# Kernel optimization log

Measured on AMD Instinct MI355X. Metric: run time of the kernel, lower is better.

The kernel has to match this reference:

```python
import jax, jax.numpy as jnp
import numpy as np

B, L, DM = 4, 2048, 1024
NL, ED, N, DTR, DCONV, SEGN = 2, 2048, 2, 64, 2, 8
SEG = max(8, round(L / SEGN))  # 256, L divisible -> all segments full


def setup_inputs():
    key = jax.random.key(0)
    ks = jax.random.split(key, 12)
    def nrm(k, sh, sc=0.02):
        return jax.random.normal(k, sh, jnp.float32) * sc
    return {
        "x": nrm(ks[0], (B, L, DM), 1.0),
        "rms_w": jnp.ones((NL, DM), jnp.float32),
        "in_w": nrm(ks[1], (NL, 2 * ED, DM)),
        "c1_w": nrm(ks[2], (NL, ED, DCONV), 0.5),
        "c1_b": jnp.zeros((NL, ED), jnp.float32),
        "c2_w": nrm(ks[3], (NL, ED, DCONV), 0.5),
        "c2_b": jnp.zeros((NL, ED), jnp.float32),
        "xp_w": nrm(ks[4], (NL, DTR + N, ED)),
        "dt_w": nrm(ks[5], (NL, ED, DTR)),
        "dt_b": jax.random.uniform(ks[6], (NL, ED), jnp.float32, -5.0, -3.0),
        "A_log": jnp.tile(jnp.log(jnp.arange(1, N + 1, dtype=jnp.float32)), (NL, ED, 1)),
        "Dp": jnp.ones((NL, ED), jnp.float32),
        "out_w": nrm(ks[7], (NL, DM, ED)),
        "k1_w": nrm(ks[8], (NL, 3 * ED, ED)),
        "k1_b": jnp.zeros((NL, 3 * ED), jnp.float32),
        "k2_w": nrm(ks[9], (NL, ED, 3 * ED)),
        "k3_w": nrm(ks[10], (NL, ED, ED)),
        "ln_g": jnp.ones((NL, ED), jnp.float32),
        "ln_b": jnp.zeros((NL, ED), jnp.float32),
        "k_alpha": jnp.zeros((NL, ED), jnp.float32),
        "sigma": jnp.full((NL,), 0.5, jnp.float32),
    }


def _dwconv(x, w, b):
    # causal depthwise conv, kernel DCONV: torch Conv1d(groups=ED, padding=DCONV-1)[..., :L]
    Lx = x.shape[1]
    xp = jnp.pad(x, ((0, 0), (DCONV - 1, 0), (0, 0)))
    y = b
    for k in range(DCONV):
        y = y + xp[:, k:k + Lx, :] * w[:, k]
    return y


def _fdu(x, dt, sigma):
    # Fourier differentiation over time axis (B, T, D)
    T = x.shape[1]
    f = jnp.fft.fftfreq(T).astype(jnp.float32)[None, :, None]
    Xf = jnp.fft.fft(x, axis=1)
    g = jnp.exp(-(f ** 2) * sigma ** 2)
    omega = 2j * jnp.pi * f / (dt + 1e-5)
    return jnp.fft.ifft(omega * (Xf * g), axis=1).real


def _kproj(e, w1, b1, w2, w3, g, bb):
    h = jax.nn.relu(e @ w1.T + b1)
    h = jax.nn.relu(h @ w2.T)
    h = h @ w3.T
    mu = jnp.mean(h, -1, keepdims=True)
    v = jnp.mean((h - mu) ** 2, -1, keepdims=True)
    return g * (h - mu) * jax.lax.rsqrt(v + 1e-5) + bb


def _pscan(a, b):
    # h_t = a_t * h_{t-1} + b_t, h_0 = b_0; (B, Lseg, ED, N)
    def comb(l, r):
        return (r[0] * l[0], r[0] * l[1] + r[1])
    return jax.lax.associative_scan(comb, (a, b), axis=1)[1]


def reference(x, rms_w, in_w, c1_w, c1_b, c2_w, c2_b, xp_w, dt_w, dt_b,
              A_log, Dp, out_w, k1_w, k1_b, k2_w, k3_w, ln_g, ln_b, k_alpha, sigma):
    h = x
    for i in range(NL):
        # RMSNorm
        xn = h * jax.lax.rsqrt(jnp.mean(h ** 2, -1, keepdims=True) + 1e-5) * rms_w[i]
        xz = xn @ in_w[i].T
        xs, z = xz[..., :ED], xz[..., ED:]
        xs = _dwconv(xs, c1_w[i], c1_b[i])
        xs = _dwconv(xs, c2_w[i], c2_b[i])
        xs = jax.nn.silu(xs)
        # ssm projections
        A = -jnp.exp(A_log[i])                       # (ED, N)
        dC = xs @ xp_w[i].T
        dr, C = dC[..., :DTR], dC[..., DTR:]
        delta = jax.nn.softplus(dr @ dt_w[i].T + dt_b[i])
        alpha = jnp.clip(k_alpha[i], 0.01, 0.99)
        yh = jnp.zeros((B, SEG, ED), xs.dtype)
        K = jnp.zeros((B, SEG, ED), xs.dtype)
        hs = []
        for s0 in range(0, L, SEG):
            xg = xs[:, s0:s0 + SEG]
            dg = delta[:, s0:s0 + SEG]
            Cg = C[:, s0:s0 + SEG]
            Kerr = jax.nn.soft_sign((xg - yh) ** 2)
            Knew = _kproj(Kerr, k1_w[i], k1_b[i], k2_w[i], k3_w[i], ln_g[i], ln_b[i])
            K = (1.0 - alpha) * K + alpha * Knew
            Kdy = K * _fdu(xg, dg, sigma[i])
            # SSOL: A_k = (A - KCA)(1 + KC), B_k = -(A - KCA) K
            Ku = K[..., None]                        # (B, Lseg, ED, 1)
            KC = Ku * Cg[:, :, None, :]              # (B, Lseg, ED, N)
            AmK = A - KC * A
            A_k = AmK * (1.0 + KC)
            B_k = -AmK * Ku
            dA = jnp.exp(dg[..., None] * A_k)
            dBx = dg[..., None] * B_k * xg[..., None] + Kdy[..., None]
            hseg = _pscan(dA, dBx)
            yh = jnp.einsum('blen,bln->ble', hseg, Cg) + Dp[i] * xg
            hs.append(hseg)
        hsall = jnp.concatenate(hs, axis=1)          # (B, L, ED, N)
        y = jnp.einsum('blen,bln->ble', hsall, C) + Dp[i] * xs
        out = (y * jax.nn.silu(z)) @ out_w[i].T
        h = h + out
    return h
```

## Files before the change

kernel.cpp:

```cpp
#include <hip/hip_runtime.h>
#include <stdint.h>


#define B_    4
#define L_    2048
#define DM_   1024
#define ED_   2048
#define SEG_  256
#define NSEG_ 8
#define CH_   16
#define TS_   16

typedef _Float16 f16x8 __attribute__((ext_vector_type(8)));
typedef _Float16 f16x4 __attribute__((ext_vector_type(4)));
typedef float    f32x4 __attribute__((ext_vector_type(4)));

__device__ __forceinline__ float siluf(float x)     { return x / (1.0f + expf(-x)); }
__device__ __forceinline__ float softplusf(float x) { return (x > 20.0f) ? x : log1pf(expf(x)); }

__global__ void f2h_kernel(const float* __restrict__ in, _Float16* __restrict__ out, int n4) {
    int i = blockIdx.x * 256 + threadIdx.x;
    if (i < n4) {
        float4 v = ((const float4*)in)[i];
        f16x4 h;
        h[0] = (_Float16)v.x; h[1] = (_Float16)v.y;
        h[2] = (_Float16)v.z; h[3] = (_Float16)v.w;
        ((f16x4*)out)[i] = h;
    }
}

__global__ __launch_bounds__(256) void rmsnorm_k(const float* __restrict__ H,
                                                 const float* __restrict__ w,
                                                 _Float16* __restrict__ out) {
    __shared__ float sred[4];
    int row = blockIdx.x;
    const float* h = H + (size_t)row * DM_;
    float ss = 0.f;
    for (int c = threadIdx.x; c < DM_; c += 256) { float v = h[c]; ss += v * v; }
    for (int off = 32; off; off >>= 1) ss += __shfl_down(ss, off, 64);
    if ((threadIdx.x & 63) == 0) sred[threadIdx.x >> 6] = ss;
    __syncthreads();
    float tot = sred[0] + sred[1] + sred[2] + sred[3];
    float scale = rsqrtf(tot * (1.0f / DM_) + 1e-5f);
    for (int c = threadIdx.x; c < DM_; c += 256)
        out[(size_t)row * DM_ + c] = (_Float16)(h[c] * scale * w[c]);
}

template<int BM, int BN, int WR, int WC, int EPI>
__global__ __launch_bounds__(256, 2)
void gemm_nt(const _Float16* __restrict__ A, const _Float16* __restrict__ Bw,
             int K, int N,
             float* outf, _Float16* __restrict__ outh, _Float16* __restrict__ outh2,
             const float* __restrict__ bias, const float* addsrc) {
    constexpr int WTM = BM / (16 * WR);
    constexpr int WTN = BN / (16 * WC);
    constexpr int NA = BM * 4 / 256;
    constexpr int NB = BN * 4 / 256;
    static_assert(BM * 4 % 256 == 0 && BN * 4 % 256 == 0, "tile");

    __shared__ __align__(16) _Float16 lsA[BM * 32];
    __shared__ __align__(16) _Float16 lsB[BN * 32];

    const int tid  = threadIdx.x;
    const int lane = tid & 63;
    const int wid  = tid >> 6;
    const int wm   = wid / WC, wn = wid % WC;
    const int m0   = blockIdx.y * BM, n0 = blockIdx.x * BN;

    f32x4 acc[WTM][WTN];
#pragma unroll
    for (int i = 0; i < WTM; ++i)
#pragma unroll
        for (int j = 0; j < WTN; ++j) acc[i][j] = (f32x4){0.f, 0.f, 0.f, 0.f};

    for (int k0 = 0; k0 < K; k0 += 32) {
        f16x8 ra[NA], rb[NB];
#pragma unroll
        for (int it = 0; it < NA; ++it) {
            int c = tid + 256 * it;
            int row = c >> 2, q = c & 3;
            int kc = q ^ ((row >> 1) & 3);
            ra[it] = *(const f16x8*)(A + (size_t)(m0 + row) * K + k0 + kc * 8);
        }
#pragma unroll
        for (int it = 0; it < NB; ++it) {
            int c = tid + 256 * it;
            int row = c >> 2, q = c & 3;
            int kc = q ^ ((row >> 1) & 3);
            rb[it] = *(const f16x8*)(Bw + (size_t)(n0 + row) * K + k0 + kc * 8);
        }
        __syncthreads();
#pragma unroll
        for (int it = 0; it < NA; ++it) { int c = tid + 256 * it; *(f16x8*)&lsA[c * 8] = ra[it]; }
#pragma unroll
        for (int it = 0; it < NB; ++it) { int c = tid + 256 * it; *(f16x8*)&lsB[c * 8] = rb[it]; }
        __syncthreads();

        f16x8 af[WTM], bfr[WTN];
#pragma unroll
        for (int i = 0; i < WTM; ++i) {
            int row = wm * (WTM * 16) + i * 16 + (lane & 15);
            int q = (lane >> 4) ^ ((row >> 1) & 3);
            af[i] = *(const f16x8*)&lsA[row * 32 + q * 8];
        }
#pragma unroll
        for (int j = 0; j < WTN; ++j) {
            int row = wn * (WTN * 16) + j * 16 + (lane & 15);
            int q = (lane >> 4) ^ ((row >> 1) & 3);
            bfr[j] = *(const f16x8*)&lsB[row * 32 + q * 8];
        }
#pragma unroll
        for (int i = 0; i < WTM; ++i)
#pragma unroll
            for (int j = 0; j < WTN; ++j)
                acc[i][j] = __builtin_amdgcn_mfma_f32_16x16x32_f16(af[i], bfr[j], acc[i][j], 0, 0, 0);
    }

#pragma unroll
    for (int i = 0; i < WTM; ++i) {
#pragma unroll
        for (int j = 0; j < WTN; ++j) {
            int mb = m0 + wm * (WTM * 16) + i * 16 + ((lane >> 4) * 4);
            int nb = n0 + wn * (WTN * 16) + j * 16 + (lane & 15);
#pragma unroll
            for (int r = 0; r < 4; ++r) {
                float v = acc[i][j][r];
                int m = mb + r;
                size_t o = (size_t)m * N + nb;
                if (EPI == 0) {
                    outf[o] = v;
                } else if (EPI == 1) {
                    int half = N >> 1;
                    if (nb < half) outh [(size_t)m * half + nb]          = (_Float16)v;
                    else           outh2[(size_t)m * half + (nb - half)] = (_Float16)v;
                } else if (EPI == 2) {
                    v += bias[nb]; v = fmaxf(v, 0.f); outh[o] = (_Float16)v;
                } else if (EPI == 3) {
                    v = fmaxf(v, 0.f); outh[o] = (_Float16)v;
                } else if (EPI == 4) {
                    outf[o] = addsrc[o] + v;
                }
            }
        }
    }
}

__global__ void convsilu_k(const _Float16* __restrict__ xp,
                           const float* __restrict__ c1w, const float* __restrict__ c1b,
                           const float* __restrict__ c2w, const float* __restrict__ c2b,
                           _Float16* __restrict__ xs, int layer) {
    size_t idx = (size_t)blockIdx.x * 256 + threadIdx.x;
    int e = (int)(idx % ED_);
    size_t bl = idx / ED_;
    int l = (int)(bl % L_);
    size_t wb = (size_t)layer * ED_ + e;
    float w10 = c1w[wb * 2], w11 = c1w[wb * 2 + 1], b1 = c1b[wb];
    float w20 = c2w[wb * 2], w21 = c2w[wb * 2 + 1], b2 = c2b[wb];
    float x0  = (float)xp[idx];
    float xm1 = (l >= 1) ? (float)xp[idx - ED_] : 0.f;
    float xm2 = (l >= 2) ? (float)xp[idx - 2 * ED_] : 0.f;
    float s1  = b1 + w10 * xm1 + w11 * x0;
    float s1m = (l >= 1) ? (b1 + w10 * xm2 + w11 * xm1) : 0.f;
    float s2  = b2 + w20 * s1m + w21 * s1;
    xs[idx] = (_Float16)siluf(s2);
}

__global__ __launch_bounds__(256) void gemv_dc(const _Float16* __restrict__ xs,
                                               const float* __restrict__ xp_w,
                                               float* __restrict__ dC, int layer) {
    int row  = blockIdx.x * 4 + (threadIdx.x >> 6);
    int lane = threadIdx.x & 63;
    const _Float16* xr = xs + (size_t)row * ED_;
    float xrow[32];
#pragma unroll
    for (int c = 0; c < 32; ++c) xrow[c] = (float)xr[c * 64 + lane];
    const float* W = xp_w + (size_t)layer * 66 * ED_;
    for (int j = 0; j < 66; ++j) {
        const float* wj = W + (size_t)j * ED_;
        float p = 0.f;
#pragma unroll
        for (int c = 0; c < 32; ++c) p += xrow[c] * wj[c * 64 + lane];
        for (int off = 32; off; off >>= 1) p += __shfl_down(p, off, 64);
        if (lane == 0) dC[(size_t)row * 66 + j] = p;
    }
}

__global__ __launch_bounds__(256) void delta_k(const float* __restrict__ dC,
                                               const float* __restrict__ dt_w,
                                               const float* __restrict__ dt_b,
                                               _Float16* __restrict__ delta, int layer) {
    __shared__ float dr[64];
    int row = blockIdx.y;
    int col = blockIdx.x * 256 + threadIdx.x;
    if (threadIdx.x < 64) dr[threadIdx.x] = dC[(size_t)row * 66 + threadIdx.x];
    __syncthreads();
    const float* w = dt_w + ((size_t)layer * ED_ + col) * 64;
    float acc = dt_b[(size_t)layer * ED_ + col];
#pragma unroll
    for (int k = 0; k < 64; k += 4) {
        float4 wv = *(const float4*)&w[k];
        acc += dr[k] * wv.x + dr[k + 1] * wv.y + dr[k + 2] * wv.z + dr[k + 3] * wv.w;
    }
    delta[(size_t)row * ED_ + col] = (_Float16)softplusf(acc);
}

__global__ void kerr_k(const _Float16* __restrict__ xs, const _Float16* __restrict__ y,
                       _Float16* __restrict__ kerr, int s0) {
    size_t idx = (size_t)blockIdx.x * 256 + threadIdx.x;
    int e = (int)(idx % ED_);
    size_t bt = idx / ED_;
    int t = (int)(bt % SEG_);
    int b = (int)(bt / SEG_);
    size_t gx = ((size_t)(b * L_ + s0 + t)) * ED_ + e;
    float xg = (float)xs[gx];
    float yh = (s0 == 0) ? 0.f : (float)y[gx - (size_t)SEG_ * ED_];
    float d = xg - yh;
    float s = d * d;
    kerr[idx] = (_Float16)(s / (1.f + s));
}

__global__ __launch_bounds__(256) void ln_ema_k(const float* __restrict__ h3,
                                                const float* __restrict__ ln_g,
                                                const float* __restrict__ ln_b,
                                                const float* __restrict__ k_alpha,
                                                float* __restrict__ K, int layer) {
    __shared__ float sred[4];
    int row = blockIdx.x;
    const float* hr = h3 + (size_t)row * ED_;
    float s = 0.f;
    for (int c = threadIdx.x; c < ED_; c += 256) s += hr[c];
    for (int off = 32; off; off >>= 1) s += __shfl_down(s, off, 64);
    if ((threadIdx.x & 63) == 0) sred[threadIdx.x >> 6] = s;
    __syncthreads();
    float mu = (sred[0] + sred[1] + sred[2] + sred[3]) * (1.0f / ED_);
    __syncthreads();
    float v = 0.f;
    for (int c = threadIdx.x; c < ED_; c += 256) { float d = hr[c] - mu; v += d * d; }
    for (int off = 32; off; off >>= 1) v += __shfl_down(v, off, 64);
    if ((threadIdx.x & 63) == 0) sred[threadIdx.x >> 6] = v;
    __syncthreads();
    float var = (sred[0] + sred[1] + sred[2] + sred[3]) * (1.0f / ED_);
    float rstd = rsqrtf(var + 1e-5f);
    for (int c = threadIdx.x; c < ED_; c += 256) {
        size_t wb = (size_t)layer * ED_ + c;
        float kn = ln_g[wb] * (hr[c] - mu) * rstd + ln_b[wb];
        float al = fminf(fmaxf(k_alpha[wb], 0.01f), 0.99f);
        size_t ki = (size_t)row * ED_ + c;
        K[ki] = (1.f - al) * K[ki] + al * kn;
    }
}

__global__ __launch_bounds__(256) void fdu_kdy_k(const _Float16* __restrict__ xs,
                                                 const _Float16* __restrict__ delta,
                                                 const float* __restrict__ K,
                                                 float* __restrict__ Kdy,
                                                 const float* __restrict__ sigma,
                                                 int layer, int s0) {
    __shared__ float re[SEG_ * 16];
    __shared__ float im[SEG_ * 16];
    __shared__ float twc[128], tws[128];
    const int tid = threadIdx.x;
    const int b   = blockIdx.x >> 7;
    const int e0  = (blockIdx.x & 127) * 16;
    float sg = sigma[layer];
    float sg2 = sg * sg;
    if (tid < 128) {
        float ang = -6.283185307179586f * (float)tid * (1.0f / 256.0f);
        twc[tid] = cosf(ang);
        tws[tid] = sinf(ang);
    }
    for (int ii = tid; ii < SEG_ * 16; ii += 256) {
        int t = ii >> 4, el = ii & 15;
        re[ii] = (float)xs[((size_t)(b * L_ + s0 + t)) * ED_ + e0 + el];
        im[ii] = 0.f;
    }
    __syncthreads();
    const int bb = tid >> 4;
    const int el = tid & 15;
#pragma unroll
    for (int ls = 7; ls >= 0; --ls) {
        int span = 1 << ls;
#pragma unroll
        for (int bi = 0; bi < 8; ++bi) {
            int bidx = bb + (bi << 4);
            int j    = bidx & (span - 1);
            int grp  = bidx >> ls;
            int p    = (grp << (ls + 1)) + j;
            int twi  = j << (7 - ls);
            int i0   = (p << 4) + el;
            int i1   = i0 + (span << 4);
            float ur = re[i0], ui = im[i0];
            float vr = re[i1], vi = im[i1];
            re[i0] = ur + vr; im[i0] = ui + vi;
            float dr = ur - vr, di = ui - vi;
            float c = twc[twi], sn = tws[twi];
            re[i1] = dr * c - di * sn;
            im[i1] = dr * sn + di * c;
        }
        __syncthreads();
    }
    for (int ii = tid; ii < SEG_ * 16; ii += 256) {
        int p = ii >> 4, ee = ii & 15;
        int k = __brev((unsigned)p) >> 24;
        float f = ((k < 128) ? (float)k : (float)(k - 256)) * (1.0f / 256.0f);
        float dt = (float)delta[((size_t)(b * L_ + s0 + k)) * ED_ + e0 + ee];
        float q = 6.283185307179586f * f * expf(-f * f * sg2) / (dt + 1e-5f);
        float xr = re[ii], xi = im[ii];
        re[ii] = -q * xi;
        im[ii] =  q * xr;
    }
    __syncthreads();
#pragma unroll
    for (int ls = 0; ls <= 7; ++ls) {
        int span = 1 << ls;
#pragma unroll
        for (int bi = 0; bi < 8; ++bi) {
            int bidx = bb + (bi << 4);
            int j    = bidx & (span - 1);
            int grp  = bidx >> ls;
            int p    = (grp << (ls + 1)) + j;
            int twi  = j << (7 - ls);
            int i0   = (p << 4) + el;
            int i1   = i0 + (span << 4);
            float c = twc[twi], sn = -tws[twi];
            float vr = re[i1], vi = im[i1];
            float tr = vr * c - vi * sn;
            float ti = vr * sn + vi * c;
            float ur = re[i0], ui = im[i0];
            re[i0] = ur + tr; im[i0] = ui + ti;
            re[i1] = ur - tr; im[i1] = ui - ti;
        }
        __syncthreads();
    }
    for (int ii = tid; ii < SEG_ * 16; ii += 256) {
        int t = ii >> 4, ee = ii & 15;
        size_t ki = ((size_t)(b * SEG_ + t)) * ED_ + e0 + ee;
        Kdy[ki] = K[ki] * re[ii] * (1.0f / 256.0f);
    }
}

__device__ __forceinline__ void scan_coefs(float dg, float xg, float Kt, float kdy,
                                           float C0, float C1, float A0, float A1,
                                           float& dA0, float& dB0, float& dA1, float& dB1) {
    float KC0 = Kt * C0;
    float AmK0 = A0 * (1.f - KC0);
    float Ak0 = AmK0 * (1.f + KC0);
    float Bk0 = -AmK0 * Kt;
    dA0 = expf(dg * Ak0);
    dB0 = dg * Bk0 * xg + kdy;
    float KC1 = Kt * C1;
    float AmK1 = A1 * (1.f - KC1);
    float Ak1 = AmK1 * (1.f + KC1);
    float Bk1 = -AmK1 * Kt;
    dA1 = expf(dg * Ak1);
    dB1 = dg * Bk1 * xg + kdy;
}

__global__ void scanA_k(const _Float16* __restrict__ delta, const _Float16* __restrict__ xs,
                        const float* __restrict__ K, const float* __restrict__ Kdy,
                        const float* __restrict__ dC, const float* __restrict__ A_log,
                        float* __restrict__ P0, float* __restrict__ P1,
                        float* __restrict__ S0, float* __restrict__ S1,
                        int layer, int s0) {
    int e = blockIdx.x * 256 + threadIdx.x;
    int b = blockIdx.y >> 4;
    int c = blockIdx.y & 15;
    float A0 = -expf(A_log[((size_t)layer * ED_ + e) * 2 + 0]);
    float A1 = -expf(A_log[((size_t)layer * ED_ + e) * 2 + 1]);
    float p0 = 1.f, p1 = 1.f, s0v = 0.f, s1v = 0.f;
    for (int tt = 0; tt < TS_; ++tt) {
        int t = c * TS_ + tt;
        size_t gi = ((size_t)(b * L_ + s0 + t)) * ED_ + e;
        size_t ki = ((size_t)(b * SEG_ + t)) * ED_ + e;
        float dg = (float)delta[gi], xg = (float)xs[gi];
        float Kt = K[ki], kdy = Kdy[ki];
        size_t ci = (size_t)(b * L_ + s0 + t) * 66 + 64;
        float C0 = dC[ci], C1 = dC[ci + 1];
        float dA0, dB0, dA1, dB1;
        scan_coefs(dg, xg, Kt, kdy, C0, C1, A0, A1, dA0, dB0, dA1, dB1);
        p0 *= dA0; s0v = dA0 * s0v + dB0;
        p1 *= dA1; s1v = dA1 * s1v + dB1;
    }
    size_t si = ((size_t)(b * CH_ + c)) * ED_ + e;
    P0[si] = p0; P1[si] = p1; S0[si] = s0v; S1[si] = s1v;
}

__global__ void scanB_k(const float* __restrict__ P0, const float* __restrict__ P1,
                        const float* __restrict__ S0, const float* __restrict__ S1,
                        float* __restrict__ Ca0, float* __restrict__ Ca1) {
    int t = blockIdx.x * 256 + threadIdx.x;
    int b = t / ED_, e = t % ED_;
    float h0 = 0.f, h1 = 0.f;
    for (int c = 0; c < CH_; ++c) {
        size_t si = ((size_t)(b * CH_ + c)) * ED_ + e;
        Ca0[si] = h0; Ca1[si] = h1;
        h0 = P0[si] * h0 + S0[si];
        h1 = P1[si] * h1 + S1[si];
    }
}

__global__ void scanC_k(const _Float16* __restrict__ delta, const _Float16* __restrict__ xs,
                        const float* __restrict__ K, const float* __restrict__ Kdy,
                        const float* __restrict__ dC, const float* __restrict__ A_log,
                        const float* __restrict__ Dp,
                        const float* __restrict__ Ca0, const float* __restrict__ Ca1,
                        _Float16* __restrict__ y, int layer, int s0) {
    int e = blockIdx.x * 256 + threadIdx.x;
    int b = blockIdx.y >> 4;
    int c = blockIdx.y & 15;
    float A0 = -expf(A_log[((size_t)layer * ED_ + e) * 2 + 0]);
    float A1 = -expf(A_log[((size_t)layer * ED_ + e) * 2 + 1]);
    float Dpe = Dp[(size_t)layer * ED_ + e];
    size_t si = ((size_t)(b * CH_ + c)) * ED_ + e;
    float h0 = Ca0[si], h1 = Ca1[si];
    for (int tt = 0; tt < TS_; ++tt) {
        int t = c * TS_ + tt;
        size_t gi = ((size_t)(b * L_ + s0 + t)) * ED_ + e;
        size_t ki = ((size_t)(b * SEG_ + t)) * ED_ + e;
        float dg = (float)delta[gi], xg = (float)xs[gi];
        float Kt = K[ki], kdy = Kdy[ki];
        size_t ci = (size_t)(b * L_ + s0 + t) * 66 + 64;
        float C0 = dC[ci], C1 = dC[ci + 1];
        float dA0, dB0, dA1, dB1;
        scan_coefs(dg, xg, Kt, kdy, C0, C1, A0, A1, dA0, dB0, dA1, dB1);
        h0 = dA0 * h0 + dB0;
        h1 = dA1 * h1 + dB1;
        y[gi] = (_Float16)(h0 * C0 + h1 * C1 + Dpe * xg);
    }
}

__global__ void gate_k(const _Float16* __restrict__ y, const _Float16* __restrict__ z,
                       _Float16* __restrict__ g) {
    size_t idx = (size_t)blockIdx.x * 256 + threadIdx.x;
    g[idx] = (_Float16)((float)y[idx] * siluf((float)z[idx]));
}

#define OFF_WK1   ((size_t)0)
#define OFF_WK2   (OFF_WK1 + 25165824)
#define OFF_WK3   (OFF_WK2 + 25165824)
#define OFF_WOUT  (OFF_WK3 + 8388608)
#define OFF_WIN   (OFF_WOUT + 4194304)
#define OFF_XN    (OFF_WIN + 8388608)
#define OFF_P     (OFF_XN + 16777216)
#define OFF_XS    (OFF_P + 33554432)
#define OFF_Z     (OFF_XS + 33554432)
#define OFF_Y     (OFF_Z + 33554432)
#define OFF_DC    (OFF_Y + 33554432)
#define OFF_H2    (OFF_DC + 2162688)
#define OFF_K     (OFF_H2 + 4194304)
#define OFF_KDY   (OFF_K + 8388608)
#define OFF_SP0   (OFF_KDY + 8388608)
#define OFF_SP1   (OFF_SP0 + 524288)
#define OFF_SS0   (OFF_SP1 + 524288)
#define OFF_SS1   (OFF_SS0 + 524288)
#define OFF_SC0   (OFF_SS1 + 524288)
#define OFF_SC1   (OFF_SC0 + 524288)
#define WS_NEED   (OFF_SC1 + 524288)

extern "C" void kernel_launch(void* const* d_in, const int* in_sizes, int n_in,
                              void* d_out, int out_size, void* d_ws, size_t ws_size,
                              hipStream_t stream) {
    if (ws_size < WS_NEED) return;

    const float* x_in   = (const float*)d_in[0];
    const float* rms_w  = (const float*)d_in[1];
    const float* in_w   = (const float*)d_in[2];
    const float* c1_w   = (const float*)d_in[3];
    const float* c1_b   = (const float*)d_in[4];
    const float* c2_w   = (const float*)d_in[5];
    const float* c2_b   = (const float*)d_in[6];
    const float* xp_w   = (const float*)d_in[7];
    const float* dt_w   = (const float*)d_in[8];
    const float* dt_b   = (const float*)d_in[9];
    const float* A_log  = (const float*)d_in[10];
    const float* Dp     = (const float*)d_in[11];
    const float* out_w  = (const float*)d_in[12];
    const float* k1_w   = (const float*)d_in[13];
    const float* k1_b   = (const float*)d_in[14];
    const float* k2_w   = (const float*)d_in[15];
    const float* k3_w   = (const float*)d_in[16];
    const float* ln_g   = (const float*)d_in[17];
    const float* ln_b   = (const float*)d_in[18];
    const float* k_alph = (const float*)d_in[19];
    const float* sigma  = (const float*)d_in[20];

    char* ws = (char*)d_ws;
    _Float16* w_k1  = (_Float16*)(ws + OFF_WK1);
    _Float16* w_k2  = (_Float16*)(ws + OFF_WK2);
    _Float16* w_k3  = (_Float16*)(ws + OFF_WK3);
    _Float16* w_out = (_Float16*)(ws + OFF_WOUT);
    _Float16* w_in  = (_Float16*)(ws + OFF_WIN);
    float*    h3buf = (float*)(ws + OFF_WIN);
    _Float16* xnbf  = (_Float16*)(ws + OFF_XN);
    _Float16* kerrb = (_Float16*)(ws + OFF_XN);
    _Float16* h1bf  = (_Float16*)(ws + OFF_XN + 4194304);
    _Float16* xs_pre= (_Float16*)(ws + OFF_P);
    _Float16* xsbuf = (_Float16*)(ws + OFF_XS);
    _Float16* zbuf  = (_Float16*)(ws + OFF_Z);
    _Float16* ybuf  = (_Float16*)(ws + OFF_Y);
    float*    dCbuf = (float*)(ws + OFF_DC);
    _Float16* h2bf  = (_Float16*)(ws + OFF_H2);
    float*    Kbuf  = (float*)(ws + OFF_K);
    float*    Kdybuf= (float*)(ws + OFF_KDY);
    float* sP0 = (float*)(ws + OFF_SP0);
    float* sP1 = (float*)(ws + OFF_SP1);
    float* sS0 = (float*)(ws + OFF_SS0);
    float* sS1 = (float*)(ws + OFF_SS1);
    float* sC0 = (float*)(ws + OFF_SC0);
    float* sC1 = (float*)(ws + OFF_SC1);
    float* dout = (float*)d_out;
    _Float16* delta = xs_pre;
    _Float16* gated = xs_pre;

    for (int layer = 0; layer < 2; ++layer) {
        hipMemsetAsync(Kbuf, 0, (size_t)B_ * SEG_ * ED_ * 4, stream);

        f2h_kernel<<<4096, 256, 0, stream>>>(in_w  + (size_t)layer * 4194304,  w_in,  1048576);
        f2h_kernel<<<12288, 256, 0, stream>>>(k1_w + (size_t)layer * 12582912, w_k1,  3145728);
        f2h_kernel<<<12288, 256, 0, stream>>>(k2_w + (size_t)layer * 12582912, w_k2,  3145728);
        f2h_kernel<<<4096, 256, 0, stream>>>(k3_w  + (size_t)layer * 4194304,  w_k3,  1048576);
        f2h_kernel<<<2048, 256, 0, stream>>>(out_w + (size_t)layer * 2097152,  w_out, 524288);

        const float* Hsrc = (layer == 0) ? x_in : dout;
        rmsnorm_k<<<B_ * L_, 256, 0, stream>>>(Hsrc, rms_w + (size_t)layer * DM_, xnbf);

        gemm_nt<128, 128, 2, 2, 1><<<dim3(32, 64), 256, 0, stream>>>(
            xnbf, w_in, 1024, 4096, nullptr, xs_pre, zbuf, nullptr, nullptr);

        convsilu_k<<<65536, 256, 0, stream>>>(xs_pre, c1_w, c1_b, c2_w, c2_b, xsbuf, layer);

        gemv_dc<<<2048, 256, 0, stream>>>(xsbuf, xp_w, dCbuf, layer);

        delta_k<<<dim3(8, 8192), 256, 0, stream>>>(dCbuf, dt_w, dt_b, delta, layer);

        for (int s = 0; s < NSEG_; ++s) {
            int s0 = s * SEG_;
            kerr_k<<<8192, 256, 0, stream>>>(xsbuf, ybuf, kerrb, s0);
            gemm_nt<128, 128, 2, 2, 2><<<dim3(48, 8), 256, 0, stream>>>(
                kerrb, w_k1, 2048, 6144, nullptr, h1bf, nullptr,
                k1_b + (size_t)layer * 6144, nullptr);
            gemm_nt<64, 128, 1, 4, 3><<<dim3(16, 16), 256, 0, stream>>>(
                h1bf, w_k2, 6144, 2048, nullptr, h2bf, nullptr, nullptr, nullptr);
            gemm_nt<64, 128, 1, 4, 0><<<dim3(16, 16), 256, 0, stream>>>(
                h2bf, w_k3, 2048, 2048, h3buf, nullptr, nullptr, nullptr, nullptr);
            ln_ema_k<<<B_ * SEG_, 256, 0, stream>>>(h3buf, ln_g, ln_b, k_alph, Kbuf, layer);
            fdu_kdy_k<<<B_ * (ED_ / 16), 256, 0, stream>>>(xsbuf, delta, Kbuf, Kdybuf,
                                                           sigma, layer, s0);
            scanA_k<<<dim3(ED_ / 256, B_ * CH_), 256, 0, stream>>>(
                delta, xsbuf, Kbuf, Kdybuf, dCbuf, A_log, sP0, sP1, sS0, sS1, layer, s0);
            scanB_k<<<(B_ * ED_) / 256, 256, 0, stream>>>(sP0, sP1, sS0, sS1, sC0, sC1);
            scanC_k<<<dim3(ED_ / 256, B_ * CH_), 256, 0, stream>>>(
                delta, xsbuf, Kbuf, Kdybuf, dCbuf, A_log, Dp, sC0, sC1, ybuf, layer, s0);
        }

        gate_k<<<65536, 256, 0, stream>>>(ybuf, zbuf, gated);
        gemm_nt<128, 128, 2, 2, 4><<<dim3(8, 64), 256, 0, stream>>>(
            gated, w_out, 2048, 1024, dout, nullptr, nullptr, nullptr,
            (layer == 0) ? x_in : dout);
    }
    (void)in_sizes; (void)n_in; (void)out_size;
}
```

Baseline: 5.573 ms.

## Use direct global-to-LDS loads in GEMM and move delta projection to MFMA GEMM

The GEMM main loop now uses global_load_lds to copy tiles straight into shared memory instead of staging them through registers. The scalar delta_k kernel is replaced by an fp16 MFMA GEMM with a new bias+softplus epilogue. gemv_dc now also writes an fp16 copy of the dt rank projection, and dt_w is converted to fp16 each layer. Removing register staging drops the register round trip but also loses the overlap of loads with the preceding compute, since there is still no double buffering. The delta path now runs in fp16 with slightly lower precision.

Result: faster. 4.846 ms (-13.0%).

```diff
diff --git a/kernel.cpp b/kernel.cpp
--- a/kernel.cpp
+++ b/kernel.cpp
@@ -17,6 +17,11 @@
 
 __device__ __forceinline__ float siluf(float x)     { return x / (1.0f + expf(-x)); }
 __device__ __forceinline__ float softplusf(float x) { return (x > 20.0f) ? x : log1pf(expf(x)); }
+
+#define GLD16(gptr, lptr)                                                     \
+    __builtin_amdgcn_global_load_lds(                                         \
+        (const __attribute__((address_space(1))) void*)(gptr),                \
+        (__attribute__((address_space(3))) void*)(lptr), 16, 0, 0)
 
 __global__ void f2h_kernel(const float* __restrict__ in, _Float16* __restrict__ out, int n4) {
     int i = blockIdx.x * 256 + threadIdx.x;
@@ -74,26 +79,21 @@
         for (int j = 0; j < WTN; ++j) acc[i][j] = (f32x4){0.f, 0.f, 0.f, 0.f};
 
     for (int k0 = 0; k0 < K; k0 += 32) {
-        f16x8 ra[NA], rb[NB];
+        __syncthreads();
 #pragma unroll
         for (int it = 0; it < NA; ++it) {
             int c = tid + 256 * it;
             int row = c >> 2, q = c & 3;
             int kc = q ^ ((row >> 1) & 3);
-            ra[it] = *(const f16x8*)(A + (size_t)(m0 + row) * K + k0 + kc * 8);
+            GLD16(A + (size_t)(m0 + row) * K + k0 + kc * 8, &lsA[c * 8]);
         }
 #pragma unroll
         for (int it = 0; it < NB; ++it) {
             int c = tid + 256 * it;
             int row = c >> 2, q = c & 3;
             int kc = q ^ ((row >> 1) & 3);
-            rb[it] = *(const f16x8*)(Bw + (size_t)(n0 + row) * K + k0 + kc * 8);
-        }
-        __syncthreads();
-#pragma unroll
-        for (int it = 0; it < NA; ++it) { int c = tid + 256 * it; *(f16x8*)&lsA[c * 8] = ra[it]; }
-#pragma unroll
-        for (int it = 0; it < NB; ++it) { int c = tid + 256 * it; *(f16x8*)&lsB[c * 8] = rb[it]; }
+            GLD16(Bw + (size_t)(n0 + row) * K + k0 + kc * 8, &lsB[c * 8]);
+        }
         __syncthreads();
 
         f16x8 af[WTM], bfr[WTN];
@@ -139,6 +139,8 @@
                     v = fmaxf(v, 0.f); outh[o] = (_Float16)v;
                 } else if (EPI == 4) {
                     outf[o] = addsrc[o] + v;
+                } else if (EPI == 5) {
+                    v += bias[nb]; outh[o] = (_Float16)softplusf(v);
                 }
             }
         }
@@ -167,7 +169,8 @@
 
 __global__ __launch_bounds__(256) void gemv_dc(const _Float16* __restrict__ xs,
                                                const float* __restrict__ xp_w,
-                                               float* __restrict__ dC, int layer) {
+                                               float* __restrict__ dC,
+                                               _Float16* __restrict__ dr16, int layer) {
     int row  = blockIdx.x * 4 + (threadIdx.x >> 6);
     int lane = threadIdx.x & 63;
     const _Float16* xr = xs + (size_t)row * ED_;
@@ -181,27 +184,11 @@
 #pragma unroll
         for (int c = 0; c < 32; ++c) p += xrow[c] * wj[c * 64 + lane];
         for (int off = 32; off; off >>= 1) p += __shfl_down(p, off, 64);
-        if (lane == 0) dC[(size_t)row * 66 + j] = p;
-    }
-}
-
-__global__ __launch_bounds__(256) void delta_k(const float* __restrict__ dC,
-                                               const float* __restrict__ dt_w,
-                                               const float* __restrict__ dt_b,
-                                               _Float16* __restrict__ delta, int layer) {
-    __shared__ float dr[64];
-    int row = blockIdx.y;
-    int col = blockIdx.x * 256 + threadIdx.x;
-    if (threadIdx.x < 64) dr[threadIdx.x] = dC[(size_t)row * 66 + threadIdx.x];
-    __syncthreads();
-    const float* w = dt_w + ((size_t)layer * ED_ + col) * 64;
-    float acc = dt_b[(size_t)layer * ED_ + col];
-#pragma unroll
-    for (int k = 0; k < 64; k += 4) {
-        float4 wv = *(const float4*)&w[k];
-        acc += dr[k] * wv.x + dr[k + 1] * wv.y + dr[k + 2] * wv.z + dr[k + 3] * wv.w;
-    }
-    delta[(size_t)row * ED_ + col] = (_Float16)softplusf(acc);
+        if (lane == 0) {
+            dC[(size_t)row * 66 + j] = p;
+            if (j < 64) dr16[(size_t)row * 64 + j] = (_Float16)p;
+        }
+    }
 }
 
 __global__ void kerr_k(const _Float16* __restrict__ xs, const _Float16* __restrict__ y,
@@ -455,7 +442,9 @@
 #define OFF_SS1   (OFF_SS0 + 524288)
 #define OFF_SC0   (OFF_SS1 + 524288)
 #define OFF_SC1   (OFF_SC0 + 524288)
-#define WS_NEED   (OFF_SC1 + 524288)
+#define OFF_WDT   (OFF_SC1 + 524288)
+#define OFF_DR16  (OFF_WDT + 262144)
+#define WS_NEED   (OFF_DR16 + 1048576)
 
 extern "C" void kernel_launch(void* const* d_in, const int* in_sizes, int n_in,
                               void* d_out, int out_size, void* d_ws, size_t ws_size,
@@ -508,6 +497,8 @@
     float* sS1 = (float*)(ws + OFF_SS1);
     float* sC0 = (float*)(ws + OFF_SC0);
     float* sC1 = (float*)(ws + OFF_SC1);
+    _Float16* w_dt  = (_Float16*)(ws + OFF_WDT);
+    _Float16* dr16  = (_Float16*)(ws + OFF_DR16);
     float* dout = (float*)d_out;
     _Float16* delta = xs_pre;
     _Float16* gated = xs_pre;
@@ -520,6 +511,7 @@
         f2h_kernel<<<12288, 256, 0, stream>>>(k2_w + (size_t)layer * 12582912, w_k2,  3145728);
         f2h_kernel<<<4096, 256, 0, stream>>>(k3_w  + (size_t)layer * 4194304,  w_k3,  1048576);
         f2h_kernel<<<2048, 256, 0, stream>>>(out_w + (size_t)layer * 2097152,  w_out, 524288);
+        f2h_kernel<<<128, 256, 0, stream>>>(dt_w  + (size_t)layer * 131072,   w_dt,  32768);
 
         const float* Hsrc = (layer == 0) ? x_in : dout;
         rmsnorm_k<<<B_ * L_, 256, 0, stream>>>(Hsrc, rms_w + (size_t)layer * DM_, xnbf);
@@ -529,9 +521,11 @@
 
         convsilu_k<<<65536, 256, 0, stream>>>(xs_pre, c1_w, c1_b, c2_w, c2_b, xsbuf, layer);
 
-        gemv_dc<<<2048, 256, 0, stream>>>(xsbuf, xp_w, dCbuf, layer);
-
-        delta_k<<<dim3(8, 8192), 256, 0, stream>>>(dCbuf, dt_w, dt_b, delta, layer);
+        gemv_dc<<<2048, 256, 0, stream>>>(xsbuf, xp_w, dCbuf, dr16, layer);
+
+        gemm_nt<128, 128, 2, 2, 5><<<dim3(16, 64), 256, 0, stream>>>(
+            dr16, w_dt, 64, 2048, nullptr, delta, nullptr,
+            dt_b + (size_t)layer * ED_, nullptr);
 
         for (int s = 0; s < NSEG_; ++s) {
             int s0 = s * SEG_;
```
